# Performance work log

Hardware: AMD Instinct MI355X
Metric: run time of the kernel (lower is better)

Reference implementation:

```python
import jax, jax.numpy as jnp
import numpy as np

N = 16384
K = 4096  # codebook_size
D = 512   # embedding_dim
COMMITMENT_COST = 0.25


def setup_inputs() -> dict:
    key = jax.random.key(0)
    kz, kc = jax.random.split(key)
    z = jax.random.normal(kz, (N, D), dtype=jnp.float32)
    # nn.Embedding weight init: uniform(-1/K, 1/K)
    codebook = jax.random.uniform(kc, (K, D), dtype=jnp.float32,
                                  minval=-1.0 / K, maxval=1.0 / K)
    return {"z": z, "codebook": codebook}


def reference(z, codebook):
    # squared L2 distances: [N, K]
    dists = (jnp.sum(z * z, axis=1, keepdims=True)
             + jnp.sum(codebook * codebook, axis=1)
             - 2.0 * jnp.matmul(z, codebook.T))
    idx = jnp.argmin(dists, axis=1)                 # [N]
    z_q = codebook[idx]                             # gather == one-hot @ codebook
    # straight-through estimator
    z_q_ste = z + jax.lax.stop_gradient(z_q - z)
    commitment_loss = jnp.mean((jax.lax.stop_gradient(z) - z_q) ** 2)
    codebook_loss = jnp.mean((z - jax.lax.stop_gradient(z_q)) ** 2)
    loss = codebook_loss + COMMITMENT_COST * commitment_loss
    encoding_indices = idx[:, None]                 # [N, 1] to match torch shape
    return (z_q_ste, encoding_indices, loss)
```

## Files before the change

kernel.cpp:

```cpp
#include <hip/hip_runtime.h>
#include <math.h>

#define N_ROWS 16384
#define K_CODES 4096
#define D_DIM 512
#define NCHUNK 8
#define KCHUNK (K_CODES / NCHUNK)
#define MARGIN 2.5e-3f
#define CCAP 32

typedef unsigned int uint32;
typedef unsigned short u16t;
typedef __attribute__((ext_vector_type(8))) short short8;
typedef __attribute__((ext_vector_type(4))) float f32x4;

__device__ __forceinline__ float fmul_(float a, float b) { return __fmul_rn(a, b); }
__device__ __forceinline__ float fadd_(float a, float b) { return __fadd_rn(a, b); }

__device__ __forceinline__ u16t f2bf(float x) {
    uint32 u = __float_as_uint(x);
    return (u16t)((u + 0x7fffu + ((u >> 16) & 1u)) >> 16);
}
__device__ __forceinline__ uint32 fkey(float f) {
    uint32 u = __float_as_uint(f);
    return (u & 0x80000000u) ? ~u : (u | 0x80000000u);
}
__device__ __forceinline__ float fdec(uint32 k) {
    uint32 u = (k & 0x80000000u) ? (k ^ 0x80000000u) : ~k;
    return __uint_as_float(u);
}
__device__ __forceinline__ float dpp_min16(float x) {
    int y;
    y = __builtin_amdgcn_update_dpp(0, __float_as_int(x), 0xB1, 0xf, 0xf, true);
    x = fminf(x, __int_as_float(y));
    y = __builtin_amdgcn_update_dpp(0, __float_as_int(x), 0x4E, 0xf, 0xf, true);
    x = fminf(x, __int_as_float(y));
    y = __builtin_amdgcn_update_dpp(0, __float_as_int(x), 0x141, 0xf, 0xf, true);
    x = fminf(x, __int_as_float(y));
    y = __builtin_amdgcn_update_dpp(0, __float_as_int(x), 0x140, 0xf, 0xf, true);
    x = fminf(x, __int_as_float(y));
    return x;
}

__global__ void prep_kernel(const float* __restrict__ z,
                            const float* __restrict__ cb,
                            u16t* __restrict__ z_bf, u16t* __restrict__ cb_bf,
                            float* __restrict__ zz, float* __restrict__ cnorm) {
    int gid = blockIdx.x * blockDim.x + threadIdx.x;
    int row = gid >> 2;
    int blk = gid & 3;
    const float* src;
    u16t* dst;
    float* outn;
    if (row < N_ROWS) {
        src = z + (size_t)row * D_DIM;
        dst = z_bf + (size_t)row * D_DIM;
        outn = zz + row;
    } else {
        int r = row - N_ROWS;
        if (r >= K_CODES) return;
        src = cb + (size_t)r * D_DIM;
        dst = cb_bf + (size_t)r * D_DIM;
        outn = cnorm + r;
    }
    const float4* p = (const float4*)(src + blk * 128);
    u16t* d = dst + blk * 128;
    float4 v0 = p[0], v1 = p[1];
    {
        short8 o;
        o[0] = (short)f2bf(v0.x); o[1] = (short)f2bf(v0.y);
        o[2] = (short)f2bf(v0.z); o[3] = (short)f2bf(v0.w);
        o[4] = (short)f2bf(v1.x); o[5] = (short)f2bf(v1.y);
        o[6] = (short)f2bf(v1.z); o[7] = (short)f2bf(v1.w);
        *(short8*)d = o;
    }
    float r0 = fmul_(v0.x, v0.x), r1 = fmul_(v0.y, v0.y);
    float r2 = fmul_(v0.z, v0.z), r3 = fmul_(v0.w, v0.w);
    float r4 = fmul_(v1.x, v1.x), r5 = fmul_(v1.y, v1.y);
    float r6 = fmul_(v1.z, v1.z), r7 = fmul_(v1.w, v1.w);
#pragma unroll
    for (int i = 1; i < 16; i++) {
        float4 w0 = p[2 * i], w1 = p[2 * i + 1];
        {
            short8 o;
            o[0] = (short)f2bf(w0.x); o[1] = (short)f2bf(w0.y);
            o[2] = (short)f2bf(w0.z); o[3] = (short)f2bf(w0.w);
            o[4] = (short)f2bf(w1.x); o[5] = (short)f2bf(w1.y);
            o[6] = (short)f2bf(w1.z); o[7] = (short)f2bf(w1.w);
            *(short8*)(d + i * 8) = o;
        }
        r0 = fadd_(r0, fmul_(w0.x, w0.x));
        r1 = fadd_(r1, fmul_(w0.y, w0.y));
        r2 = fadd_(r2, fmul_(w0.z, w0.z));
        r3 = fadd_(r3, fmul_(w0.w, w0.w));
        r4 = fadd_(r4, fmul_(w1.x, w1.x));
        r5 = fadd_(r5, fmul_(w1.y, w1.y));
        r6 = fadd_(r6, fmul_(w1.z, w1.z));
        r7 = fadd_(r7, fmul_(w1.w, w1.w));
    }
    float s = fadd_(fadd_(fadd_(r0, r1), fadd_(r2, r3)),
                    fadd_(fadd_(r4, r5), fadd_(r6, r7)));
    float u = __shfl_down(s, 1, 64);
    float t = fadd_(s, u);
    float w = __shfl_down(t, 2, 64);
    float tot = fadd_(t, w);
    if (blk == 0) *outn = tot;
}

__global__ void rownorm_np_kernel(const float* __restrict__ src, int nrows,
                                  float* __restrict__ out) {
    int gid = blockIdx.x * blockDim.x + threadIdx.x;
    int row = gid >> 2;
    int blk = gid & 3;
    if (row >= nrows) return;
    const float4* p = (const float4*)(src + (size_t)row * D_DIM + blk * 128);
    float4 v0 = p[0], v1 = p[1];
    float r0 = fmul_(v0.x, v0.x), r1 = fmul_(v0.y, v0.y);
    float r2 = fmul_(v0.z, v0.z), r3 = fmul_(v0.w, v0.w);
    float r4 = fmul_(v1.x, v1.x), r5 = fmul_(v1.y, v1.y);
    float r6 = fmul_(v1.z, v1.z), r7 = fmul_(v1.w, v1.w);
#pragma unroll
    for (int i = 1; i < 16; i++) {
        float4 w0 = p[2 * i], w1 = p[2 * i + 1];
        r0 = fadd_(r0, fmul_(w0.x, w0.x));
        r1 = fadd_(r1, fmul_(w0.y, w0.y));
        r2 = fadd_(r2, fmul_(w0.z, w0.z));
        r3 = fadd_(r3, fmul_(w0.w, w0.w));
        r4 = fadd_(r4, fmul_(w1.x, w1.x));
        r5 = fadd_(r5, fmul_(w1.y, w1.y));
        r6 = fadd_(r6, fmul_(w1.z, w1.z));
        r7 = fadd_(r7, fmul_(w1.w, w1.w));
    }
    float s = fadd_(fadd_(fadd_(r0, r1), fadd_(r2, r3)),
                    fadd_(fadd_(r4, r5), fadd_(r6, r7)));
    float u = __shfl_down(s, 1, 64);
    float t = fadd_(s, u);
    float w = __shfl_down(t, 2, 64);
    float tot = fadd_(t, w);
    if (blk == 0) out[row] = tot;
}

__global__ __launch_bounds__(512, 4) void score_gemm_kernel(
    const u16t* __restrict__ zb, const u16t* __restrict__ cbb,
    const float* __restrict__ cnorm,
    float* __restrict__ chunkmin,
    uint32* __restrict__ cnts,
    uint2* __restrict__ cand) {
    __shared__ alignas(16) u16t Ab[128 * 64];
    __shared__ alignas(16) u16t Bb[128 * 64];
    __shared__ uint32 rowminU[128];
    __shared__ int ccnt[128];

    const int t = threadIdx.x;
    const int panel = blockIdx.x;
    const int chunk = blockIdx.y;
    const int row0 = panel * 128, k0 = chunk * KCHUNK;
    const int w = t >> 6, lane = t & 63;
    const int wx = w & 1, wy = w >> 1;
    const int l15 = lane & 15, quad = lane >> 4;

    if (t < 128) { rowminU[t] = 0xFFFFFFFFu; ccnt[t] = 0; }

    for (int kt = 0; kt < 4; kt++) {
        f32x4 acc[2][4];
#pragma unroll
        for (int i = 0; i < 2; i++)
#pragma unroll
            for (int j = 0; j < 4; j++) acc[i][j] = (f32x4){0.f, 0.f, 0.f, 0.f};

        const u16t* ga = zb + (size_t)(row0 + (t >> 2)) * D_DIM + (t & 3) * 8;
        const u16t* gb = cbb + (size_t)(k0 + kt * 128 + (t >> 2)) * D_DIM + (t & 3) * 8;

        for (int dt = 0; dt < 8; dt++) {
            __syncthreads();
            __builtin_amdgcn_global_load_lds(
                (const __attribute__((address_space(1))) void*)ga,
                (__attribute__((address_space(3))) void*)((char*)Ab + w * 1024),
                16, 0, 0);
            __builtin_amdgcn_global_load_lds(
                (const __attribute__((address_space(1))) void*)(ga + 32),
                (__attribute__((address_space(3))) void*)((char*)Ab + 8192 + w * 1024),
                16, 0, 0);
            __builtin_amdgcn_global_load_lds(
                (const __attribute__((address_space(1))) void*)gb,
                (__attribute__((address_space(3))) void*)((char*)Bb + w * 1024),
                16, 0, 0);
            __builtin_amdgcn_global_load_lds(
                (const __attribute__((address_space(1))) void*)(gb + 32),
                (__attribute__((address_space(3))) void*)((char*)Bb + 8192 + w * 1024),
                16, 0, 0);
            ga += 64; gb += 64;
            __syncthreads();
#pragma unroll
            for (int sub = 0; sub < 2; sub++) {
                short8 a[2];
#pragma unroll
                for (int i = 0; i < 2; i++)
                    a[i] = *(const short8*)((char*)Ab + sub * 8192 +
                                            (wy * 32 + i * 16 + l15) * 64 + quad * 16);
#pragma unroll
                for (int j = 0; j < 4; j++) {
                    short8 b = *(const short8*)((char*)Bb + sub * 8192 +
                                                (wx * 64 + j * 16 + l15) * 64 + quad * 16);
#pragma unroll
                    for (int i = 0; i < 2; i++)
                        acc[i][j] = __builtin_amdgcn_mfma_f32_16x16x32_bf16(a[i], b, acc[i][j], 0, 0, 0);
                }
            }
        }

        float cnj[4];
#pragma unroll
        for (int j = 0; j < 4; j++)
            cnj[j] = cnorm[k0 + kt * 128 + wx * 64 + j * 16 + l15];

#pragma unroll
        for (int i = 0; i < 2; i++) {
#pragma unroll
            for (int r = 0; r < 4; r++) {
                float m = fmaf(-2.f, acc[i][0][r], cnj[0]);
                m = fminf(m, fmaf(-2.f, acc[i][1][r], cnj[1]));
                m = fminf(m, fmaf(-2.f, acc[i][2][r], cnj[2]));
                m = fminf(m, fmaf(-2.f, acc[i][3][r], cnj[3]));
                m = dpp_min16(m);
                if (l15 == 0)
                    atomicMin(&rowminU[wy * 32 + i * 16 + quad * 4 + r], fkey(m));
            }
        }
        __syncthreads();
#pragma unroll
        for (int i = 0; i < 2; i++) {
#pragma unroll
            for (int r = 0; r < 4; r++) {
                const int rl = wy * 32 + i * 16 + quad * 4 + r;
                const float thr = fdec(rowminU[rl]) + MARGIN;
#pragma unroll
                for (int j = 0; j < 4; j++) {
                    float s = fmaf(-2.f, acc[i][j][r], cnj[j]);
                    if (s <= thr) {
                        int pos = atomicAdd(&ccnt[rl], 1);
                        if (pos < CCAP) {
                            uint2 e;
                            e.x = __float_as_uint(s);
                            e.y = (uint32)(k0 + kt * 128 + wx * 64 + j * 16 + l15);
                            cand[((size_t)(row0 + rl) * NCHUNK + chunk) * CCAP + pos] = e;
                        }
                    }
                }
            }
        }
    }
    __syncthreads();
    if (t < 128) {
        chunkmin[(size_t)(row0 + t) * NCHUNK + chunk] = fdec(rowminU[t]);
        int c = ccnt[t];
        cnts[(size_t)(row0 + t) * NCHUNK + chunk] = (uint32)(c < CCAP ? c : CCAP);
    }
}

__global__ __launch_bounds__(256) void refine_kernel(
    const uint2* __restrict__ cand, const uint32* __restrict__ cnts,
    const float* __restrict__ chunkmin,
    const float* __restrict__ z, const float* __restrict__ cb,
    const float* __restrict__ zz, const float* __restrict__ cnorm,
    float* __restrict__ out_zq, float* __restrict__ out_idx,
    float* __restrict__ rowsum) {
    const int t = threadIdx.x;
    const int wid = t >> 6, lane = t & 63;
    const int row = blockIdx.x * 4 + wid;

    float cm = chunkmin[(size_t)row * NCHUNK + (lane & 7)];
    cm = fminf(cm, __shfl_xor(cm, 1, 64));
    cm = fminf(cm, __shfl_xor(cm, 2, 64));
    cm = fminf(cm, __shfl_xor(cm, 4, 64));
    const float thr = cm + MARGIN;

    const float* zr = z + (size_t)row * D_DIM;
    float4 z0 = *(const float4*)(zr + lane * 8);
    float4 z1 = *(const float4*)(zr + lane * 8 + 4);
    const float zzr = zz[row];

    float bv = 3.4e38f;
    int bi = 0x7fffffff;
#pragma unroll
    for (int it = 0; it < (NCHUNK * CCAP) / 64; ++it) {
        int idx = it * 64 + lane;
        int c = idx >> 5, s2 = idx & (CCAP - 1);
        uint32 n = cnts[(size_t)row * NCHUNK + c];
        int kk = -1;
        if ((uint32)s2 < n) {
            uint2 e = cand[((size_t)row * NCHUNK + c) * CCAP + s2];
            if (__uint_as_float(e.x) <= thr) kk = (int)e.y;
        }
        unsigned long long mask = __ballot(kk >= 0);
        while (mask) {
            int src = __ffsll((unsigned long long)mask) - 1;
            mask &= (mask - 1);
            int k = __shfl(kk, src, 64);
            const float* cr = cb + (size_t)k * D_DIM;
            float4 c0 = *(const float4*)(cr + lane * 8);
            float4 c1 = *(const float4*)(cr + lane * 8 + 4);
            float d = fmul_(z0.x, c0.x);
            d = fmaf(z0.y, c0.y, d); d = fmaf(z0.z, c0.z, d); d = fmaf(z0.w, c0.w, d);
            d = fmaf(z1.x, c1.x, d); d = fmaf(z1.y, c1.y, d);
            d = fmaf(z1.z, c1.z, d); d = fmaf(z1.w, c1.w, d);
#pragma unroll
            for (int off = 1; off < 64; off <<= 1)
                d = fadd_(d, __shfl_xor(d, off, 64));
            float dist = fmaf(-2.f, d, fadd_(zzr, cnorm[k]));
            if (dist < bv || (dist == bv && k < bi)) { bv = dist; bi = k; }
        }
    }
    if (bi == 0x7fffffff) bi = 0;
    if (lane == 0) out_idx[row] = (float)bi;

    const float* cq = cb + (size_t)bi * D_DIM;
    float v[4];
#pragma unroll
    for (int q = 0; q < 4; q++) {
        const int off = q * 128 + lane * 2;
        float2 zv2 = *(const float2*)(zr + off);
        float2 cv2 = *(const float2*)(cq + off);
        float2 o;
        o.x = fadd_(zv2.x, __fsub_rn(cv2.x, zv2.x));
        o.y = fadd_(zv2.y, __fsub_rn(cv2.y, zv2.y));
        *(float2*)(out_zq + (size_t)row * D_DIM + off) = o;
        float dx = zv2.x - cv2.x, dy = zv2.y - cv2.y;
        v[q] = dx * dx + dy * dy;
    }
    float s = fadd_(fadd_(v[0], v[2]), fadd_(v[1], v[3]));
    s = fadd_(s, __shfl_down(s, 32, 64));
    s = fadd_(s, __shfl_down(s, 16, 64));
    s = fadd_(s, __shfl_down(s, 8, 64));
    s = fadd_(s, __shfl_down(s, 4, 64));
    s = fadd_(s, __shfl_down(s, 2, 64));
    s = fadd_(s, __shfl_down(s, 1, 64));
    if (lane == 0) rowsum[row] = s;
}

__global__ void loss_kernel(const float* __restrict__ rowsum,
                            float* __restrict__ out_loss) {
    __shared__ float sm[256];
    float s = 0.f;
    for (int i = threadIdx.x; i < N_ROWS; i += 256) s += rowsum[i];
    sm[threadIdx.x] = s;
    __syncthreads();
    for (int st = 128; st; st >>= 1) {
        if (threadIdx.x < st) sm[threadIdx.x] += sm[threadIdx.x + st];
        __syncthreads();
    }
    if (threadIdx.x == 0)
        *out_loss = 1.25f * sm[0] / (float)(N_ROWS * D_DIM);
}

#define BM 128
#define BN 128
#define BK 16
#define TM 8
#define TN 8

__global__ __launch_bounds__(256, 4) void vq_argmin_kernel(
    const float* __restrict__ z, const float* __restrict__ cb,
    const float* __restrict__ zz, const float* __restrict__ cnorm,
    float* __restrict__ pval, int* __restrict__ pidx) {
    __shared__ float As[BK][BM + 4];
    __shared__ float Bs[BK][BN + 4];
    __shared__ float rv[BM][17];
    __shared__ int   ri[BM][17];

    const int bx = blockIdx.x;
    const int by = blockIdx.y;
    const int row0 = by * BM;
    const int k0 = bx * KCHUNK;
    const int t = threadIdx.x;
    const int tx = t & 15;
    const int ty = t >> 4;

    float minv[TM];
    int   mini[TM];
#pragma unroll
    for (int i = 0; i < TM; i++) { minv[i] = 3.4e38f; mini[i] = 0; }
    float zrow[TM];
#pragma unroll
    for (int i = 0; i < TM; i++) zrow[i] = zz[row0 + ty * TM + i];
    const int sr = t >> 1;
    const int sdq = (t & 1) * 8;

    for (int kt = 0; kt < KCHUNK / BN; kt++) {
        const int col0 = k0 + kt * BN;
        float acc[TM][TN];
#pragma unroll
        for (int i = 0; i < TM; i++)
#pragma unroll
            for (int j = 0; j < TN; j++) acc[i][j] = 0.f;
        for (int dt = 0; dt < D_DIM; dt += BK) {
            {
                const float* src = z + (size_t)(row0 + sr) * D_DIM + dt + sdq;
                float4 v0 = *(const float4*)(src);
                float4 v1 = *(const float4*)(src + 4);
                As[sdq + 0][sr] = v0.x; As[sdq + 1][sr] = v0.y;
                As[sdq + 2][sr] = v0.z; As[sdq + 3][sr] = v0.w;
                As[sdq + 4][sr] = v1.x; As[sdq + 5][sr] = v1.y;
                As[sdq + 6][sr] = v1.z; As[sdq + 7][sr] = v1.w;
                const float* srcb = cb + (size_t)(col0 + sr) * D_DIM + dt + sdq;
                float4 w0 = *(const float4*)(srcb);
                float4 w1 = *(const float4*)(srcb + 4);
                Bs[sdq + 0][sr] = w0.x; Bs[sdq + 1][sr] = w0.y;
                Bs[sdq + 2][sr] = w0.z; Bs[sdq + 3][sr] = w0.w;
                Bs[sdq + 4][sr] = w1.x; Bs[sdq + 5][sr] = w1.y;
                Bs[sdq + 6][sr] = w1.z; Bs[sdq + 7][sr] = w1.w;
            }
            __syncthreads();
#pragma unroll
            for (int d = 0; d < BK; d++) {
                float a[TM], b[TN];
#pragma unroll
                for (int i = 0; i < TM; i++) a[i] = As[d][ty * TM + i];
#pragma unroll
                for (int j = 0; j < TN; j++) b[j] = Bs[d][tx * TN + j];
#pragma unroll
                for (int i = 0; i < TM; i++)
#pragma unroll
                    for (int j = 0; j < TN; j++)
                        acc[i][j] = fmaf(a[i], b[j], acc[i][j]);
            }
            __syncthreads();
        }
#pragma unroll
        for (int j = 0; j < TN; j++) {
            const int col = col0 + tx * TN + j;
            const float cn = cnorm[col];
#pragma unroll
            for (int i = 0; i < TM; i++) {
                float s1 = fadd_(zrow[i], cn);
                float s = fmaf(-2.f, acc[i][j], s1);
                if (s < minv[i]) { minv[i] = s; mini[i] = col; }
            }
        }
    }
#pragma unroll
    for (int i = 0; i < TM; i++) {
        rv[ty * TM + i][tx] = minv[i];
        ri[ty * TM + i][tx] = mini[i];
    }
    __syncthreads();
    if (t < BM) {
        float bv = rv[t][0];
        int   bi = ri[t][0];
#pragma unroll
        for (int x = 1; x < 16; x++) {
            float v = rv[t][x]; int ii = ri[t][x];
            if (v < bv || (v == bv && ii < bi)) { bv = v; bi = ii; }
        }
        pval[(size_t)(row0 + t) * NCHUNK + bx] = bv;
        pidx[(size_t)(row0 + t) * NCHUNK + bx] = bi;
    }
}

__global__ void finalize_kernel(const float* __restrict__ z,
                                const float* __restrict__ cb,
                                const float* __restrict__ pval,
                                const int* __restrict__ pidx,
                                float* __restrict__ out_zq,
                                float* __restrict__ out_idx,
                                float* __restrict__ rowsum) {
    int row = (blockIdx.x * blockDim.x + threadIdx.x) >> 6;
    int lane = threadIdx.x & 63;
    if (row >= N_ROWS) return;
    float bv = pval[(size_t)row * NCHUNK];
    int   bi = pidx[(size_t)row * NCHUNK];
#pragma unroll
    for (int c = 1; c < NCHUNK; c++) {
        float v = pval[(size_t)row * NCHUNK + c];
        int  ii = pidx[(size_t)row * NCHUNK + c];
        if (v < bv || (v == bv && ii < bi)) { bv = v; bi = ii; }
    }
    const float4* zr = (const float4*)(z + (size_t)row * D_DIM);
    const float4* cr = (const float4*)(cb + (size_t)bi * D_DIM);
    float4* orow = (float4*)(out_zq + (size_t)row * D_DIM);
    float s = 0.f;
#pragma unroll
    for (int i = 0; i < 2; i++) {
        float4 zv = zr[i * 64 + lane];
        float4 cv = cr[i * 64 + lane];
        float4 o;
        o.x = fadd_(zv.x, __fsub_rn(cv.x, zv.x));
        o.y = fadd_(zv.y, __fsub_rn(cv.y, zv.y));
        o.z = fadd_(zv.z, __fsub_rn(cv.z, zv.z));
        o.w = fadd_(zv.w, __fsub_rn(cv.w, zv.w));
        orow[i * 64 + lane] = o;
        float dx = zv.x - cv.x, dy = zv.y - cv.y;
        float dz = zv.z - cv.z, dw = zv.w - cv.w;
        s += dx * dx + dy * dy + dz * dz + dw * dw;
    }
#pragma unroll
    for (int off = 32; off; off >>= 1) s += __shfl_down(s, off, 64);
    if (lane == 0) {
        rowsum[row] = s;
        out_idx[row] = (float)bi;
    }
}

extern "C" void kernel_launch(void* const* d_in, const int* in_sizes, int n_in,
                              void* d_out, int out_size, void* d_ws, size_t ws_size,
                              hipStream_t stream) {
    const float* z  = (const float*)d_in[0];
    const float* cb = (const float*)d_in[1];
    float* out      = (float*)d_out;
    float* out_zq   = out;
    float* out_idx  = out + (size_t)N_ROWS * D_DIM;
    float* out_loss = out_idx + N_ROWS;

    float* zz     = (float*)d_ws;
    float* cnorm  = zz + N_ROWS;
    float* rowsum = cnorm + K_CODES;
    u16t*  z_bf   = (u16t*)(rowsum + N_ROWS);
    u16t*  cb_bf  = z_bf + (size_t)N_ROWS * D_DIM;
    float* chunkmin = (float*)(cb_bf + (size_t)K_CODES * D_DIM);
    uint32* cnts  = (uint32*)(chunkmin + (size_t)N_ROWS * NCHUNK);
    uint2* cand   = (uint2*)(cnts + (size_t)N_ROWS * NCHUNK);
    const size_t WS_NEEDED = (size_t)(N_ROWS + K_CODES + N_ROWS) * 4
                           + (size_t)N_ROWS * D_DIM * 2
                           + (size_t)K_CODES * D_DIM * 2
                           + (size_t)N_ROWS * NCHUNK * 4 * 2
                           + (size_t)N_ROWS * NCHUNK * CCAP * 8;

    if (ws_size >= WS_NEEDED) {
        prep_kernel<<<((N_ROWS + K_CODES) * 4) / 256, 256, 0, stream>>>(
            z, cb, z_bf, cb_bf, zz, cnorm);

        dim3 g1(N_ROWS / 128, NCHUNK);
        score_gemm_kernel<<<g1, 512, 0, stream>>>(z_bf, cb_bf, cnorm,
                                                  chunkmin, cnts, cand);
        refine_kernel<<<N_ROWS / 4, 256, 0, stream>>>(cand, cnts, chunkmin,
                                                      z, cb, zz, cnorm,
                                                      out_zq, out_idx, rowsum);
        loss_kernel<<<1, 256, 0, stream>>>(rowsum, out_loss);
    } else {
        float* pval = rowsum + N_ROWS;
        int*   pidx = (int*)(pval + (size_t)N_ROWS * NCHUNK);
        rownorm_np_kernel<<<(N_ROWS * 4) / 256, 256, 0, stream>>>(z, N_ROWS, zz);
        rownorm_np_kernel<<<(K_CODES * 4) / 256, 256, 0, stream>>>(cb, K_CODES, cnorm);
        dim3 g2(NCHUNK, N_ROWS / BM);
        vq_argmin_kernel<<<g2, 256, 0, stream>>>(z, cb, zz, cnorm, pval, pidx);
        finalize_kernel<<<N_ROWS / 4, 256, 0, stream>>>(z, cb, pval, pidx,
                                                        out_zq, out_idx, rowsum);
        loss_kernel<<<1, 256, 0, stream>>>(rowsum, out_loss);
    }
}
```

Baseline: 262.1 us.

## Double-buffer LDS tiles in score GEMM with vmcnt-based prefetch

```diff
diff --git a/kernel.cpp b/kernel.cpp
--- a/kernel.cpp
+++ b/kernel.cpp
@@ -140,14 +140,30 @@
     if (blk == 0) out[row] = tot;
 }
 
+#define STAGE4(gaP, gbP, bufA, bufB)                                        \
+    do {                                                                    \
+        __builtin_amdgcn_global_load_lds(                                   \
+            (const __attribute__((address_space(1))) void*)(gaP),           \
+            (__attribute__((address_space(3))) void*)((char*)(bufA) + w * 1024), 16, 0, 0); \
+        __builtin_amdgcn_global_load_lds(                                   \
+            (const __attribute__((address_space(1))) void*)((gaP) + 32),    \
+            (__attribute__((address_space(3))) void*)((char*)(bufA) + 8192 + w * 1024), 16, 0, 0); \
+        __builtin_amdgcn_global_load_lds(                                   \
+            (const __attribute__((address_space(1))) void*)(gbP),           \
+            (__attribute__((address_space(3))) void*)((char*)(bufB) + w * 1024), 16, 0, 0); \
+        __builtin_amdgcn_global_load_lds(                                   \
+            (const __attribute__((address_space(1))) void*)((gbP) + 32),    \
+            (__attribute__((address_space(3))) void*)((char*)(bufB) + 8192 + w * 1024), 16, 0, 0); \
+    } while (0)
+
 __global__ __launch_bounds__(512, 4) void score_gemm_kernel(
     const u16t* __restrict__ zb, const u16t* __restrict__ cbb,
     const float* __restrict__ cnorm,
     float* __restrict__ chunkmin,
     uint32* __restrict__ cnts,
     uint2* __restrict__ cand) {
-    __shared__ alignas(16) u16t Ab[128 * 64];
-    __shared__ alignas(16) u16t Bb[128 * 64];
+    __shared__ alignas(16) u16t Ab[2][128 * 64];
+    __shared__ alignas(16) u16t Bb[2][128 * 64];
     __shared__ uint32 rowminU[128];
     __shared__ int ccnt[128];
 
@@ -171,41 +187,35 @@
         const u16t* ga = zb + (size_t)(row0 + (t >> 2)) * D_DIM + (t & 3) * 8;
         const u16t* gb = cbb + (size_t)(k0 + kt * 128 + (t >> 2)) * D_DIM + (t & 3) * 8;
 
+        STAGE4(ga, gb, Ab[0], Bb[0]);  ga += 64; gb += 64;
+        STAGE4(ga, gb, Ab[1], Bb[1]);  ga += 64; gb += 64;
+
         for (int dt = 0; dt < 8; dt++) {
-            __syncthreads();
-            __builtin_amdgcn_global_load_lds(
-                (const __attribute__((address_space(1))) void*)ga,
-                (__attribute__((address_space(3))) void*)((char*)Ab + w * 1024),
-                16, 0, 0);
-            __builtin_amdgcn_global_load_lds(
-                (const __attribute__((address_space(1))) void*)(ga + 32),
-                (__attribute__((address_space(3))) void*)((char*)Ab + 8192 + w * 1024),
-                16, 0, 0);
-            __builtin_amdgcn_global_load_lds(
-                (const __attribute__((address_space(1))) void*)gb,
-                (__attribute__((address_space(3))) void*)((char*)Bb + w * 1024),
-                16, 0, 0);
-            __builtin_amdgcn_global_load_lds(
-                (const __attribute__((address_space(1))) void*)(gb + 32),
-                (__attribute__((address_space(3))) void*)((char*)Bb + 8192 + w * 1024),
-                16, 0, 0);
-            ga += 64; gb += 64;
-            __syncthreads();
+            const int cur = dt & 1;
+            if (dt < 7) asm volatile("s_waitcnt vmcnt(4)" ::: "memory");
+            else        asm volatile("s_waitcnt vmcnt(0)" ::: "memory");
+            __builtin_amdgcn_s_barrier();
+            __builtin_amdgcn_sched_barrier(0);
 #pragma unroll
             for (int sub = 0; sub < 2; sub++) {
                 short8 a[2];
 #pragma unroll
                 for (int i = 0; i < 2; i++)
-                    a[i] = *(const short8*)((char*)Ab + sub * 8192 +
+                    a[i] = *(const short8*)((char*)Ab[cur] + sub * 8192 +
                                             (wy * 32 + i * 16 + l15) * 64 + quad * 16);
 #pragma unroll
                 for (int j = 0; j < 4; j++) {
-                    short8 b = *(const short8*)((char*)Bb + sub * 8192 +
+                    short8 b = *(const short8*)((char*)Bb[cur] + sub * 8192 +
                                                 (wx * 64 + j * 16 + l15) * 64 + quad * 16);
 #pragma unroll
                     for (int i = 0; i < 2; i++)
                         acc[i][j] = __builtin_amdgcn_mfma_f32_16x16x32_bf16(a[i], b, acc[i][j], 0, 0, 0);
                 }
+            }
+            __builtin_amdgcn_s_barrier();
+            __builtin_amdgcn_sched_barrier(0);
+            if (dt < 6) {
+                STAGE4(ga, gb, Ab[cur], Bb[cur]);  ga += 64; gb += 64;
             }
         }
 
```

Result: no change. 257.5 us (-1.8%).
